# Optimization experiments

Hardware: AMD Instinct MI355X
Metric: run time of the kernel (lower is better)

## Reference

```python
import jax, jax.numpy as jnp
import numpy as np

EPS = 1e-8


def _entropy_1d(p):
    # entropy() helper with input_as_probabilities=True on a 1-D tensor:
    # clamp to EPS, x*log(x), return -sum
    p_ = jnp.maximum(p, EPS)
    return -jnp.sum(p_ * jnp.log(p_))


def setup_inputs() -> dict:
    key = jax.random.key(0)
    k1, k2 = jax.random.split(key)
    b, n = 65536, 512
    anchors = jax.random.normal(k1, (b, n), dtype=jnp.float32)
    neighbors = jax.random.normal(k2, (b, n), dtype=jnp.float32)
    return {"anchors": anchors, "neighbors": neighbors}


def reference(anchors, neighbors):
    entropy_weight = 2.0
    b, n = anchors.shape

    anchors_prob = jax.nn.softmax(anchors, axis=1)      # [b, n]
    positives_prob = jax.nn.softmax(neighbors, axis=1)  # [b, n]

    # bmm of [b,1,n] x [b,n,1] -> row-wise dot product, shape [b]
    similarity = jnp.einsum('bn,bn->b', anchors_prob, positives_prob)

    # BCELoss(similarity, ones) = -mean(log(sim)); torch clamps log at -100
    consistency_loss = -jnp.mean(jnp.maximum(jnp.log(similarity), -100.0))

    lg_sim = jnp.log(similarity)

    entropy_loss = _entropy_1d(jnp.mean(anchors_prob, axis=0))

    # cross/second-order: dot of clamped sim with clamped log-sim
    second_order_loss = jnp.dot(jnp.maximum(similarity, EPS),
                                jnp.maximum(lg_sim, EPS))

    # np.tile(sim, n).reshape(n, b) then view(b, n, 1): equivalent to the
    # flat [b*n] tiled vector reshaped row-major to [b, n]
    tiled_sim = jnp.tile(similarity, n).reshape(b, n)
    third_order_entropy = jnp.einsum('bn,bn->b', anchors_prob, tiled_sim)
    lg_third = jnp.log(third_order_entropy)
    third_order_loss = jnp.dot(jnp.maximum(third_order_entropy, EPS),
                               jnp.maximum(lg_third, EPS)) / n

    third_weight = 0.5 / np.sqrt(n)
    diff_weight = 0.25 / n

    total_loss = (consistency_loss
                  - entropy_weight * entropy_loss
                  + diff_weight * second_order_loss
                  - third_weight * third_order_loss)
    return (total_loss, consistency_loss, entropy_loss,
            second_order_loss, third_order_loss)
```

## Files before the change

### kernel.cpp

```cpp
#include <hip/hip_runtime.h>
#include <math.h>

#define B_ROWS 65536
#define N_COLS 512
#define EPS 1e-8f
#define NREP 8
#define GRID1 2048
#define GRID2 2048


__device__ __forceinline__ float wave_reduce_sum(float v) {
#pragma unroll
    for (int m = 32; m >= 1; m >>= 1) v += __shfl_xor(v, m, 64);
    return v;
}

__global__ __launch_bounds__(256) void scan_pass1(
        const float* __restrict__ A, const float* __restrict__ Bn,
        float* __restrict__ sim, float* __restrict__ colsum,
        float* __restrict__ acc) {
    __shared__ float cs[512];
    __shared__ float slog[4];
    __shared__ float ssec[4];

    const int t    = threadIdx.x;
    const int lane = t & 63;
    const int wv   = t >> 6;
    const int wave = (blockIdx.x * blockDim.x + t) >> 6;
    const int nw   = (GRID1 * 256) >> 6;

    float cacc[8];
#pragma unroll
    for (int k = 0; k < 8; ++k) cacc[k] = 0.f;
    float accLog = 0.f, accSec = 0.f;

    int i = wave;
    const float* a = A  + (size_t)i * N_COLS + lane * 4;
    const float* b = Bn + (size_t)i * N_COLS + lane * 4;
    float4 a0 = *(const float4*)(a);
    float4 a1 = *(const float4*)(a + 256);
    float4 b0 = *(const float4*)(b);
    float4 b1 = *(const float4*)(b + 256);

    while (i < B_ROWS) {
        const int inext = i + nw;
        float4 na0, na1, nb0, nb1;
        if (inext < B_ROWS) {
            const float* an = A  + (size_t)inext * N_COLS + lane * 4;
            const float* bn = Bn + (size_t)inext * N_COLS + lane * 4;
            na0 = *(const float4*)(an);
            na1 = *(const float4*)(an + 256);
            nb0 = *(const float4*)(bn);
            nb1 = *(const float4*)(bn + 256);
        }

        float av[8] = {a0.x, a0.y, a0.z, a0.w, a1.x, a1.y, a1.z, a1.w};
        float bv[8] = {b0.x, b0.y, b0.z, b0.w, b1.x, b1.y, b1.z, b1.w};

        float ea[8];
        float sa = 0.f, sb = 0.f, dp = 0.f;
#pragma unroll
        for (int k = 0; k < 8; ++k) {
            ea[k]    = __expf(av[k]);
            float eb = __expf(bv[k]);
            sa += ea[k];
            sb += eb;
            dp += ea[k] * eb;
        }
        sa = wave_reduce_sum(sa);
        sb = wave_reduce_sum(sb);
        dp = wave_reduce_sum(dp);

        float inv_sa = 1.f / sa;
        float s = dp * inv_sa * (1.f / sb);
#pragma unroll
        for (int k = 0; k < 8; ++k) cacc[k] += ea[k] * inv_sa;

        if (lane == 0) {
            sim[i] = s;
            float lg = __logf(s);
            accLog += fmaxf(lg, -100.f);
            accSec += fmaxf(s, EPS) * fmaxf(lg, EPS);
        }

        a0 = na0; a1 = na1; b0 = nb0; b1 = nb1;
        i = inext;
    }

    cs[t] = 0.f; cs[t + 256] = 0.f;
    __syncthreads();
#pragma unroll
    for (int k = 0; k < 4; ++k) atomicAdd(&cs[lane * 4 + k], cacc[k]);
#pragma unroll
    for (int k = 0; k < 4; ++k) atomicAdd(&cs[256 + lane * 4 + k], cacc[4 + k]);
    if (lane == 0) { slog[wv] = accLog; ssec[wv] = accSec; }
    __syncthreads();
    float* crep = colsum + (blockIdx.x & (NREP - 1)) * 512;
    atomicAdd(&crep[t], cs[t]);
    atomicAdd(&crep[t + 256], cs[t + 256]);
    if (t == 0) {
        atomicAdd(&acc[0], slog[0] + slog[1] + slog[2] + slog[3]);
        atomicAdd(&acc[1], ssec[0] + ssec[1] + ssec[2] + ssec[3]);
    }
}

__global__ __launch_bounds__(256) void scan_pass2(
        const float* __restrict__ A, const float* __restrict__ sim,
        float* __restrict__ acc) {
    __shared__ float sthird[4];
    const int t    = threadIdx.x;
    const int lane = t & 63;
    const int wv   = t >> 6;
    const int wave = (blockIdx.x * blockDim.x + t) >> 6;
    const int nw   = (GRID2 * 256) >> 6;

    float accThird = 0.f;

    int i = wave;
    const float* a = A + (size_t)i * N_COLS + lane * 4;
    const float* s = sim + (size_t)(i & 127) * N_COLS + lane * 4;
    float4 a0 = *(const float4*)(a);
    float4 a1 = *(const float4*)(a + 256);
    float4 s0 = *(const float4*)(s);
    float4 s1 = *(const float4*)(s + 256);

    while (i < B_ROWS) {
        const int inext = i + nw;
        float4 na0, na1;
        if (inext < B_ROWS) {
            const float* an = A + (size_t)inext * N_COLS + lane * 4;
            na0 = *(const float4*)(an);
            na1 = *(const float4*)(an + 256);
        }

        float av[8] = {a0.x, a0.y, a0.z, a0.w, a1.x, a1.y, a1.z, a1.w};
        float sv[8] = {s0.x, s0.y, s0.z, s0.w, s1.x, s1.y, s1.z, s1.w};

        float sa = 0.f, dp = 0.f;
#pragma unroll
        for (int k = 0; k < 8; ++k) {
            float e = __expf(av[k]);
            sa += e;
            dp += e * sv[k];
        }
        sa = wave_reduce_sum(sa);
        dp = wave_reduce_sum(dp);

        if (lane == 0) {
            float toe = dp / sa;
            float lg  = __logf(toe);
            accThird += fmaxf(toe, EPS) * fmaxf(lg, EPS);
        }

        a0 = na0; a1 = na1;
        i = inext;
    }
    if (lane == 0) sthird[wv] = accThird;
    __syncthreads();
    if (t == 0)
        atomicAdd(&acc[2], sthird[0] + sthird[1] + sthird[2] + sthird[3]);
}

__global__ __launch_bounds__(64) void scan_finalize(
        const float* __restrict__ colsum, const float* __restrict__ acc,
        float* __restrict__ out) {
    const int lane = threadIdx.x;
    float e = 0.f;
#pragma unroll
    for (int k = 0; k < 8; ++k) {
        const int col = lane * 8 + k;
        float c = 0.f;
#pragma unroll
        for (int r = 0; r < NREP; ++r) c += colsum[r * 512 + col];
        float p = c * (1.f / B_ROWS);
        p = fmaxf(p, EPS);
        e -= p * __logf(p);
    }
#pragma unroll
    for (int m = 32; m >= 1; m >>= 1) e += __shfl_xor(e, m, 64);
    if (lane == 0) {
        float consistency = -acc[0] * (1.f / B_ROWS);
        float second      = acc[1];
        float third       = acc[2] * (1.f / N_COLS);
        float entropy     = e;
        float third_weight = 0.5f / sqrtf((float)N_COLS);
        float diff_weight  = 0.25f / (float)N_COLS;
        float total = consistency - 2.0f * entropy + diff_weight * second
                      - third_weight * third;
        out[0] = total;
        out[1] = consistency;
        out[2] = entropy;
        out[3] = second;
        out[4] = third;
    }
}

extern "C" void kernel_launch(void* const* d_in, const int* in_sizes, int n_in,
                              void* d_out, int out_size, void* d_ws, size_t ws_size,
                              hipStream_t stream) {
    const float* anchors   = (const float*)d_in[0];
    const float* neighbors = (const float*)d_in[1];
    float* out = (float*)d_out;

    float* sim    = (float*)d_ws;
    float* colsum = sim + B_ROWS;
    float* acc    = colsum + NREP * 512;

    hipMemsetAsync(colsum, 0, (NREP * 512 + 4) * sizeof(float), stream);

    scan_pass1<<<dim3(GRID1), dim3(256), 0, stream>>>(anchors, neighbors, sim, colsum, acc);
    scan_pass2<<<dim3(GRID2), dim3(256), 0, stream>>>(anchors, sim, acc);
    scan_finalize<<<1, 64, 0, stream>>>(colsum, acc, out);
}
```

Before: 341.4 us.

## Map four rows per wave with 16-lane row groups and unrolled loads

Each wave now processes four rows at once, with 16 lanes per row and two fixed iterations instead of a grid-stride loop with explicit prefetch. Each lane issues eight float4 loads per tensor up front, and the cross-lane reductions shrink to four shuffle steps. Pass 2 loads its sim slab once for both iterations. The aim is more memory-level parallelism and fewer shuffles, at the cost of many more registers (32 column accumulators) and more LDS atomics.

```diff
diff --git a/kernel.cpp b/kernel.cpp
--- a/kernel.cpp
+++ b/kernel.cpp
@@ -9,156 +9,151 @@
 #define GRID2 2048
 
 
-__device__ __forceinline__ float wave_reduce_sum(float v) {
-#pragma unroll
-    for (int m = 32; m >= 1; m >>= 1) v += __shfl_xor(v, m, 64);
-    return v;
-}
-
 __global__ __launch_bounds__(256) void scan_pass1(
         const float* __restrict__ A, const float* __restrict__ Bn,
         float* __restrict__ sim, float* __restrict__ colsum,
         float* __restrict__ acc) {
     __shared__ float cs[512];
-    __shared__ float slog[4];
-    __shared__ float ssec[4];
+    __shared__ float sred[8];
 
     const int t    = threadIdx.x;
     const int lane = t & 63;
-    const int wv   = t >> 6;
-    const int wave = (blockIdx.x * blockDim.x + t) >> 6;
-    const int nw   = (GRID1 * 256) >> 6;
-
-    float cacc[8];
-#pragma unroll
-    for (int k = 0; k < 8; ++k) cacc[k] = 0.f;
+    const int sub  = lane & 15;
+    const int g    = lane >> 4;
+    const int wave = (blockIdx.x * 256 + t) >> 6;
+
+    float cacc[32];
+#pragma unroll
+    for (int k = 0; k < 32; ++k) cacc[k] = 0.f;
     float accLog = 0.f, accSec = 0.f;
 
-    int i = wave;
-    const float* a = A  + (size_t)i * N_COLS + lane * 4;
-    const float* b = Bn + (size_t)i * N_COLS + lane * 4;
-    float4 a0 = *(const float4*)(a);
-    float4 a1 = *(const float4*)(a + 256);
-    float4 b0 = *(const float4*)(b);
-    float4 b1 = *(const float4*)(b + 256);
-
-    while (i < B_ROWS) {
-        const int inext = i + nw;
-        float4 na0, na1, nb0, nb1;
-        if (inext < B_ROWS) {
-            const float* an = A  + (size_t)inext * N_COLS + lane * 4;
-            const float* bn = Bn + (size_t)inext * N_COLS + lane * 4;
-            na0 = *(const float4*)(an);
-            na1 = *(const float4*)(an + 256);
-            nb0 = *(const float4*)(bn);
-            nb1 = *(const float4*)(bn + 256);
-        }
-
-        float av[8] = {a0.x, a0.y, a0.z, a0.w, a1.x, a1.y, a1.z, a1.w};
-        float bv[8] = {b0.x, b0.y, b0.z, b0.w, b1.x, b1.y, b1.z, b1.w};
-
-        float ea[8];
+#pragma unroll
+    for (int iter = 0; iter < 2; ++iter) {
+        const int row = wave * 4 + g + iter * 32768;
+        const float* a = A  + (size_t)row * N_COLS;
+        const float* b = Bn + (size_t)row * N_COLS;
+
+        float4 av4[8], bv4[8];
+#pragma unroll
+        for (int k = 0; k < 8; ++k) {
+            av4[k] = *(const float4*)(a + (k * 16 + sub) * 4);
+            bv4[k] = *(const float4*)(b + (k * 16 + sub) * 4);
+        }
+
+        float ea[32];
         float sa = 0.f, sb = 0.f, dp = 0.f;
 #pragma unroll
         for (int k = 0; k < 8; ++k) {
-            ea[k]    = __expf(av[k]);
-            float eb = __expf(bv[k]);
-            sa += ea[k];
-            sb += eb;
-            dp += ea[k] * eb;
-        }
-        sa = wave_reduce_sum(sa);
-        sb = wave_reduce_sum(sb);
-        dp = wave_reduce_sum(dp);
+            float avv[4] = {av4[k].x, av4[k].y, av4[k].z, av4[k].w};
+            float bvv[4] = {bv4[k].x, bv4[k].y, bv4[k].z, bv4[k].w};
+#pragma unroll
+            for (int c = 0; c < 4; ++c) {
+                float e = __expf(avv[c]);
+                float f = __expf(bvv[c]);
+                ea[k * 4 + c] = e;
+                sa += e; sb += f; dp += e * f;
+            }
+        }
+
+#pragma unroll
+        for (int m = 8; m >= 1; m >>= 1) {
+            sa += __shfl_xor(sa, m, 64);
+            sb += __shfl_xor(sb, m, 64);
+            dp += __shfl_xor(dp, m, 64);
+        }
 
         float inv_sa = 1.f / sa;
-        float s = dp * inv_sa * (1.f / sb);
-#pragma unroll
-        for (int k = 0; k < 8; ++k) cacc[k] += ea[k] * inv_sa;
-
-        if (lane == 0) {
-            sim[i] = s;
+#pragma unroll
+        for (int k = 0; k < 32; ++k) cacc[k] += ea[k] * inv_sa;
+
+        if (sub == 0) {
+            float s = dp * inv_sa * (1.f / sb);
+            sim[row] = s;
             float lg = __logf(s);
             accLog += fmaxf(lg, -100.f);
             accSec += fmaxf(s, EPS) * fmaxf(lg, EPS);
         }
-
-        a0 = na0; a1 = na1; b0 = nb0; b1 = nb1;
-        i = inext;
-    }
+    }
+
+    accLog += __shfl_xor(accLog, 16, 64); accLog += __shfl_xor(accLog, 32, 64);
+    accSec += __shfl_xor(accSec, 16, 64); accSec += __shfl_xor(accSec, 32, 64);
 
     cs[t] = 0.f; cs[t + 256] = 0.f;
     __syncthreads();
 #pragma unroll
-    for (int k = 0; k < 4; ++k) atomicAdd(&cs[lane * 4 + k], cacc[k]);
-#pragma unroll
-    for (int k = 0; k < 4; ++k) atomicAdd(&cs[256 + lane * 4 + k], cacc[4 + k]);
-    if (lane == 0) { slog[wv] = accLog; ssec[wv] = accSec; }
+    for (int k = 0; k < 8; ++k)
+#pragma unroll
+        for (int c = 0; c < 4; ++c)
+            atomicAdd(&cs[64 * k + 4 * sub + c], cacc[k * 4 + c]);
+    if (lane == 0) { sred[(t >> 6)] = accLog; sred[4 + (t >> 6)] = accSec; }
     __syncthreads();
+
     float* crep = colsum + (blockIdx.x & (NREP - 1)) * 512;
     atomicAdd(&crep[t], cs[t]);
     atomicAdd(&crep[t + 256], cs[t + 256]);
-    if (t == 0) {
-        atomicAdd(&acc[0], slog[0] + slog[1] + slog[2] + slog[3]);
-        atomicAdd(&acc[1], ssec[0] + ssec[1] + ssec[2] + ssec[3]);
-    }
+    if (t == 0)
+        atomicAdd(&acc[0], sred[0] + sred[1] + sred[2] + sred[3]);
+    if (t == 1)
+        atomicAdd(&acc[1], sred[4] + sred[5] + sred[6] + sred[7]);
 }
 
 __global__ __launch_bounds__(256) void scan_pass2(
         const float* __restrict__ A, const float* __restrict__ sim,
         float* __restrict__ acc) {
-    __shared__ float sthird[4];
+    __shared__ float sred[4];
     const int t    = threadIdx.x;
     const int lane = t & 63;
-    const int wv   = t >> 6;
-    const int wave = (blockIdx.x * blockDim.x + t) >> 6;
-    const int nw   = (GRID2 * 256) >> 6;
+    const int sub  = lane & 15;
+    const int g    = lane >> 4;
+    const int wave = (blockIdx.x * 256 + t) >> 6;
+
+    const int slab = (wave * 4 + g) & 127;
+    const float* sp = sim + (size_t)slab * N_COLS;
+    float4 sv4[8];
+#pragma unroll
+    for (int k = 0; k < 8; ++k)
+        sv4[k] = *(const float4*)(sp + (k * 16 + sub) * 4);
 
     float accThird = 0.f;
-
-    int i = wave;
-    const float* a = A + (size_t)i * N_COLS + lane * 4;
-    const float* s = sim + (size_t)(i & 127) * N_COLS + lane * 4;
-    float4 a0 = *(const float4*)(a);
-    float4 a1 = *(const float4*)(a + 256);
-    float4 s0 = *(const float4*)(s);
-    float4 s1 = *(const float4*)(s + 256);
-
-    while (i < B_ROWS) {
-        const int inext = i + nw;
-        float4 na0, na1;
-        if (inext < B_ROWS) {
-            const float* an = A + (size_t)inext * N_COLS + lane * 4;
-            na0 = *(const float4*)(an);
-            na1 = *(const float4*)(an + 256);
-        }
-
-        float av[8] = {a0.x, a0.y, a0.z, a0.w, a1.x, a1.y, a1.z, a1.w};
-        float sv[8] = {s0.x, s0.y, s0.z, s0.w, s1.x, s1.y, s1.z, s1.w};
+#pragma unroll
+    for (int iter = 0; iter < 2; ++iter) {
+        const int row = wave * 4 + g + iter * 32768;
+        const float* a = A + (size_t)row * N_COLS;
+        float4 av4[8];
+#pragma unroll
+        for (int k = 0; k < 8; ++k)
+            av4[k] = *(const float4*)(a + (k * 16 + sub) * 4);
 
         float sa = 0.f, dp = 0.f;
 #pragma unroll
         for (int k = 0; k < 8; ++k) {
-            float e = __expf(av[k]);
-            sa += e;
-            dp += e * sv[k];
-        }
-        sa = wave_reduce_sum(sa);
-        dp = wave_reduce_sum(dp);
-
-        if (lane == 0) {
+            float avv[4] = {av4[k].x, av4[k].y, av4[k].z, av4[k].w};
+            float svv[4] = {sv4[k].x, sv4[k].y, sv4[k].z, sv4[k].w};
+#pragma unroll
+            for (int c = 0; c < 4; ++c) {
+                float e = __expf(avv[c]);
+                sa += e;
+                dp += e * svv[c];
+            }
+        }
+#pragma unroll
+        for (int m = 8; m >= 1; m >>= 1) {
+            sa += __shfl_xor(sa, m, 64);
+            dp += __shfl_xor(dp, m, 64);
+        }
+        if (sub == 0) {
             float toe = dp / sa;
             float lg  = __logf(toe);
             accThird += fmaxf(toe, EPS) * fmaxf(lg, EPS);
         }
-
-        a0 = na0; a1 = na1;
-        i = inext;
-    }
-    if (lane == 0) sthird[wv] = accThird;
+    }
+
+    accThird += __shfl_xor(accThird, 16, 64);
+    accThird += __shfl_xor(accThird, 32, 64);
+    if (lane == 0) sred[t >> 6] = accThird;
     __syncthreads();
     if (t == 0)
-        atomicAdd(&acc[2], sthird[0] + sthird[1] + sthird[2] + sthird[3]);
+        atomicAdd(&acc[2], sred[0] + sred[1] + sred[2] + sred[3]);
 }
 
 __global__ __launch_bounds__(64) void scan_finalize(
```

New measurement: 350.9 us. +2.8%, slower.
